# Kernel tuning notes

Hardware: AMD Instinct MI355X
Metric: run time of the kernel (lower is better)

## Reference

```python
import jax, jax.numpy as jnp
import numpy as np

EMBED_DIM = 1024
NUM_HEADS = 16
HEAD_DIM = EMBED_DIM // NUM_HEADS
B, L = 2, 2048
SCALE = HEAD_DIM ** -0.5


def setup_inputs() -> dict:
    key = jax.random.key(0)
    ks = jax.random.split(key, 8)
    x = jax.random.normal(ks[0], (B, L, EMBED_DIM), dtype=jnp.float32)
    phylo_dists = jax.random.uniform(ks[1], (B, L), dtype=jnp.float32)
    alibi_bias = jax.random.normal(ks[2], (NUM_HEADS, L, L), dtype=jnp.float32) * 0.02
    # causal mask: 1 where attending allowed (j <= i), broadcast over B,H
    attn_mask = (jnp.arange(L)[:, None] >= jnp.arange(L)[None, :])[None, None]
    # learned params (Linear stores weight as [out, in]; y = x @ W.T + b)
    qkv_w = jax.random.normal(ks[3], (3 * EMBED_DIM, EMBED_DIM), dtype=jnp.float32) * (EMBED_DIM ** -0.5)
    qkv_b = jnp.zeros((3 * EMBED_DIM,), dtype=jnp.float32)
    out_w = jax.random.normal(ks[4], (EMBED_DIM, EMBED_DIM), dtype=jnp.float32) * (EMBED_DIM ** -0.5)
    out_b = jnp.zeros((EMBED_DIM,), dtype=jnp.float32)
    phylo_alpha = jnp.float32(0.5)
    return {"x": x, "phylo_dists": phylo_dists, "alibi_bias": alibi_bias,
            "attn_mask": attn_mask, "qkv_w": qkv_w, "qkv_b": qkv_b,
            "out_w": out_w, "out_b": out_b, "phylo_alpha": phylo_alpha}


def reference(x, phylo_dists, alibi_bias, attn_mask, qkv_w, qkv_b, out_w, out_b, phylo_alpha):
    Bm, Lm, D = x.shape
    qkv = (x @ qkv_w.T + qkv_b).reshape(Bm, Lm, 3, NUM_HEADS, HEAD_DIM)
    qkv = jnp.transpose(qkv, (2, 0, 3, 1, 4))  # [3, B, H, L, hd]
    q, k, v = qkv[0], qkv[1], qkv[2]
    # phylo temperature: scalar per batch element
    phylo_scalar = phylo_dists.mean(axis=-1).reshape(Bm, 1, 1, 1)
    temp = jnp.clip(1.0 + phylo_alpha * phylo_scalar, 1e-6, None)
    scores = jnp.einsum('bhqd,bhkd->bhqk', q, k) * (SCALE * temp)
    scores = scores + alibi_bias[None]  # [B,H,L,L]
    scores = jnp.where(attn_mask, scores, -jnp.inf)
    attn = jax.nn.softmax(scores, axis=-1)
    out = jnp.einsum('bhqk,bhkd->bhqd', attn, v)
    out = jnp.transpose(out, (0, 2, 1, 3)).reshape(Bm, Lm, D)
    return out @ out_w.T + out_b
```

## Files before the change

### kernel.cpp

```cpp
#include <hip/hip_runtime.h>
#include <hip/hip_bf16.h>

typedef __attribute__((ext_vector_type(8))) short bf16x8;
typedef __attribute__((ext_vector_type(4))) float f32x4;
typedef __attribute__((ext_vector_type(4))) float f4v;
typedef __attribute__((ext_vector_type(4))) short s4v;

__device__ __forceinline__ short f2bf(float f) {
    union { __hip_bfloat16 h; short s; } u;
    u.h = __float2bfloat16(f);
    return u.s;
}

__device__ __forceinline__ void gload_lds16(const void* g, void* l) {
    __builtin_amdgcn_global_load_lds(
        (const __attribute__((address_space(1))) void*)g,
        (__attribute__((address_space(3))) void*)l,
        16, 0, 0);
}

#define MFMA16(a, b, c) __builtin_amdgcn_mfma_f32_16x16x32_bf16((a), (b), (c), 0, 0, 0)

__global__ void prep_kernel(const float* __restrict__ x,
                            const float* __restrict__ qw,
                            const float* __restrict__ ow,
                            const float* __restrict__ pd,
                            const float* __restrict__ alphap,
                            s4v* __restrict__ xb, s4v* __restrict__ qb,
                            s4v* __restrict__ ob, float* __restrict__ scales) {
    __shared__ float wsum[4];
    if (blockIdx.x >= 2048) {
        int b = blockIdx.x - 2048;
        float s = 0.f;
        for (int i = threadIdx.x; i < 2048; i += 256) s += pd[b * 2048 + i];
        for (int o = 32; o; o >>= 1) s += __shfl_down(s, o);
        if ((threadIdx.x & 63) == 0) wsum[threadIdx.x >> 6] = s;
        __syncthreads();
        if (threadIdx.x == 0) {
            float t = wsum[0] + wsum[1] + wsum[2] + wsum[3];
            float mean = t * (1.0f / 2048.0f);
            float temp = fmaxf(1.0f + alphap[0] * mean, 1e-6f);
            scales[b] = 0.125f * temp;
        }
        return;
    }
    #pragma unroll
    for (int j = 0; j < 4; ++j) {
        int idx = blockIdx.x * 1024 + j * 256 + threadIdx.x;
        const f4v* src;
        s4v* dst;
        int off;
        if (idx < 1048576)      { src = (const f4v*)x;  dst = xb; off = idx; }
        else if (idx < 1835008) { src = (const f4v*)qw; dst = qb; off = idx - 1048576; }
        else                    { src = (const f4v*)ow; dst = ob; off = idx - 1835008; }
        f4v v = src[off];
        s4v o;
        #pragma unroll
        for (int k = 0; k < 4; ++k) o[k] = f2bf(v[k]);
        dst[off] = o;
    }
}

__global__ __launch_bounds__(512, 2)
void gemm_qkv_8ph(const __hip_bfloat16* __restrict__ A,
                  const __hip_bfloat16* __restrict__ Bw,
                  const float* __restrict__ bias,
                  __hip_bfloat16* __restrict__ C) {
    extern __shared__ short lds[];
    const int tid = threadIdx.x;
    const int wave = tid >> 6, lane = tid & 63;
    const int g = lane >> 4, c = lane & 15;
    const int wr = wave >> 2, wc = wave & 3;

    int bid = blockIdx.y * 12 + blockIdx.x;
    bid = (bid & 7) * 24 + (bid >> 3);
    const long m0 = (long)(bid / 12) * 256;
    const long n0 = (long)(bid % 12) * 256;

    const int sr = tid >> 3;
    const int ss = tid & 7;
    const int sl = ss ^ (sr & 7);
    const int srowoff = 2 * sr + (sl >> 2);
    const int skel = (sl & 3) * 8;

    const int xterm = (((c & 1) << 6) | (g << 4)) ^ ((c >> 1) << 4);

    f32x4 acc[8][4];
    #pragma unroll
    for (int m = 0; m < 8; ++m)
        #pragma unroll
        for (int n = 0; n < 4; ++n) acc[m][n] = f32x4{0.f, 0.f, 0.f, 0.f};

#define STAGE_A(tt, d)                                                        \
    {                                                                         \
        _Pragma("unroll")                                                     \
        for (int h = 0; h < 2; ++h) {                                         \
            const __hip_bfloat16* src =                                       \
                A + (m0 + h * 128 + srowoff) * 1024 + (tt) * 32 + skel;       \
            gload_lds16(src, lds + (d) * 16384 + (h * 512 + tid) * 8);        \
        }                                                                     \
    }
#define STAGE_B(tt, d)                                                        \
    {                                                                         \
        _Pragma("unroll")                                                     \
        for (int h = 0; h < 2; ++h) {                                         \
            const __hip_bfloat16* src =                                       \
                Bw + (n0 + h * 128 + srowoff) * 1024 + (tt) * 32 + skel;      \
            gload_lds16(src, lds + (d) * 16384 + 8192 + (h * 512 + tid) * 8); \
        }                                                                     \
    }

    STAGE_A(0, 0); STAGE_B(0, 0);
    STAGE_A(1, 1); STAGE_B(1, 1);
    asm volatile("s_waitcnt vmcnt(4)" ::: "memory");
    __builtin_amdgcn_s_barrier();

    const int NT = 32;
    for (int t = 0; t < NT; ++t) {
        const int d = t % 3;
        const char* bufA = (const char*)(lds + d * 16384);
        const char* bufB = (const char*)(lds + d * 16384 + 8192);
        const int dn = (t + 2) % 3;
        const bool st = (t + 2 < NT);

        bf16x8 af[8], bfr0, bfr1;
        #pragma unroll
        for (int m = 0; m < 8; ++m) {
            int row = wr * 64 + m * 8 + (c >> 1);
            af[m] = *(const bf16x8*)(bufA + row * 128 + xterm);
        }
        {
            int row0 = wc * 32 + 0 * 8 + (c >> 1);
            int row1 = wc * 32 + 1 * 8 + (c >> 1);
            bfr0 = *(const bf16x8*)(bufB + row0 * 128 + xterm);
            bfr1 = *(const bf16x8*)(bufB + row1 * 128 + xterm);
        }
        if (st) STAGE_A(t + 2, dn);
        __builtin_amdgcn_s_barrier();
        asm volatile("s_waitcnt lgkmcnt(0)" ::: "memory");
        __builtin_amdgcn_sched_barrier(0);
        __builtin_amdgcn_s_setprio(1);
        #pragma unroll
        for (int m = 0; m < 8; ++m) {
            acc[m][0] = MFMA16(af[m], bfr0, acc[m][0]);
            acc[m][1] = MFMA16(af[m], bfr1, acc[m][1]);
        }
        __builtin_amdgcn_s_setprio(0);
        __builtin_amdgcn_s_barrier();

        {
            int row2 = wc * 32 + 2 * 8 + (c >> 1);
            int row3 = wc * 32 + 3 * 8 + (c >> 1);
            bfr0 = *(const bf16x8*)(bufB + row2 * 128 + xterm);
            bfr1 = *(const bf16x8*)(bufB + row3 * 128 + xterm);
        }
        if (st) STAGE_B(t + 2, dn);
        __builtin_amdgcn_s_barrier();
        if (t < NT - 2)
            asm volatile("s_waitcnt vmcnt(4)" ::: "memory");
        else if (t == NT - 2)
            asm volatile("s_waitcnt vmcnt(0)" ::: "memory");
        asm volatile("s_waitcnt lgkmcnt(0)" ::: "memory");
        __builtin_amdgcn_sched_barrier(0);
        __builtin_amdgcn_s_setprio(1);
        #pragma unroll
        for (int m = 0; m < 8; ++m) {
            acc[m][2] = MFMA16(af[m], bfr0, acc[m][2]);
            acc[m][3] = MFMA16(af[m], bfr1, acc[m][3]);
        }
        __builtin_amdgcn_s_setprio(0);
        __builtin_amdgcn_s_barrier();
    }
#undef STAGE_A
#undef STAGE_B

    #pragma unroll
    for (int m = 0; m < 8; ++m) {
        #pragma unroll
        for (int n = 0; n < 4; ++n) {
            long col = n0 + wc * 64 + n * 16 + c;
            float bv = bias[col];
            #pragma unroll
            for (int r = 0; r < 4; ++r) {
                long row = m0 + wr * 128 + m * 16 + g * 4 + r;
                C[row * 3072 + col] = __float2bfloat16(acc[m][n][r] + bv);
            }
        }
    }
}

template<int BF16_OUT, int NF>
__global__ __launch_bounds__(256, 2)
void gemm_nt(const __hip_bfloat16* __restrict__ A,
             const __hip_bfloat16* __restrict__ Bw,
             const float* __restrict__ bias,
             void* __restrict__ Cv,
             int M, int N, int K) {
    __shared__ short sA[128 * 64];
    __shared__ short sB[NF * 32 * 64];
    const int tid = threadIdx.x;
    const int wave = tid >> 6, lane = tid & 63;
    const int g = lane >> 4, c = lane & 15;
    const int wr = wave >> 1, wc = wave & 1;
    const long m0 = (long)blockIdx.y * 128, n0 = (long)blockIdx.x * (NF * 32);

    f32x4 acc[4][NF];
    #pragma unroll
    for (int m = 0; m < 4; ++m)
        #pragma unroll
        for (int n = 0; n < NF; ++n) acc[m][n] = f32x4{0.f, 0.f, 0.f, 0.f};

    for (int k0 = 0; k0 < K; k0 += 64) {
        #pragma unroll
        for (int i = 0; i < 4; ++i) {
            int cb = (i * 4 + wave) * 64;
            int chunk = cb + lane;
            int row = chunk >> 3;
            int sc = ((chunk & 7) * 16) ^ ((row & 7) << 4);
            const char* gA = (const char*)(A + (m0 + row) * (long)K + k0) + sc;
            gload_lds16(gA, (char*)sA + cb * 16);
        }
        #pragma unroll
        for (int i = 0; i < NF; ++i) {
            int cb = (i * 4 + wave) * 64;
            int chunk = cb + lane;
            int row = chunk >> 3;
            int sc = ((chunk & 7) * 16) ^ ((row & 7) << 4);
            const char* gB = (const char*)(Bw + (n0 + row) * (long)K + k0) + sc;
            gload_lds16(gB, (char*)sB + cb * 16);
        }
        __syncthreads();
        #pragma unroll
        for (int s = 0; s < 2; ++s) {
            bf16x8 af[4], bfr[NF];
            #pragma unroll
            for (int m = 0; m < 4; ++m) {
                int row = wr * 64 + m * 16 + c;
                int kb = (s * 64 + g * 16) ^ ((row & 7) << 4);
                af[m] = *(const bf16x8*)((const char*)sA + row * 128 + kb);
            }
            #pragma unroll
            for (int n = 0; n < NF; ++n) {
                int row = wc * (NF * 16) + n * 16 + c;
                int kb = (s * 64 + g * 16) ^ ((row & 7) << 4);
                bfr[n] = *(const bf16x8*)((const char*)sB + row * 128 + kb);
            }
            #pragma unroll
            for (int m = 0; m < 4; ++m)
                #pragma unroll
                for (int n = 0; n < NF; ++n)
                    acc[m][n] = MFMA16(af[m], bfr[n], acc[m][n]);
        }
        __syncthreads();
    }

    #pragma unroll
    for (int m = 0; m < 4; ++m) {
        #pragma unroll
        for (int n = 0; n < NF; ++n) {
            long col = n0 + wc * (NF * 16) + n * 16 + c;
            float bv = bias[col];
            #pragma unroll
            for (int r = 0; r < 4; ++r) {
                long row = m0 + wr * 64 + m * 16 + g * 4 + r;
                float v = acc[m][n][r] + bv;
                if (BF16_OUT)
                    ((__hip_bfloat16*)Cv)[row * N + col] = __float2bfloat16(v);
                else
                    ((float*)Cv)[row * N + col] = v;
            }
        }
    }
}

__device__ __forceinline__ void compute_tile(
    const bf16x8 (&kf)[4][2], const short* sVtc, short* sPw,
    bf16x8 qf0, bf16x8 qf1,
    f32x4 (&acc_o)[4], f32x4& accL, float (&m)[4],
    const float (&ab)[4][4],
    float scale, int qi0, int kv0, bool diag, int g, int c)
{
    f32x4 accs[4];
    __builtin_amdgcn_s_setprio(1);
    #pragma unroll
    for (int nf = 0; nf < 4; ++nf) {
        accs[nf] = f32x4{0.f, 0.f, 0.f, 0.f};
        accs[nf] = MFMA16(qf0, kf[nf][0], accs[nf]);
        accs[nf] = MFMA16(qf1, kf[nf][1], accs[nf]);
    }
    __builtin_amdgcn_s_setprio(0);
    float s[4][4], pmax[4];
    bool ok = true;
    #pragma unroll
    for (int r = 0; r < 4; ++r) {
        int qi = qi0 + r;
        #pragma unroll
        for (int nf = 0; nf < 4; ++nf) {
            float sv = fmaf(accs[nf][r], scale, ab[nf][r]);
            if (diag && (kv0 + nf * 16 + c > qi)) sv = -1e30f;
            s[r][nf] = sv;
        }
        pmax[r] = fmaxf(fmaxf(s[r][0], s[r][1]), fmaxf(s[r][2], s[r][3]));
        ok = ok && (pmax[r] <= m[r] + 8.0f);
    }
    if (!__all(ok)) {
        #pragma unroll
        for (int r = 0; r < 4; ++r) {
            float mx = pmax[r];
            mx = fmaxf(mx, __shfl_xor(mx, 1));
            mx = fmaxf(mx, __shfl_xor(mx, 2));
            mx = fmaxf(mx, __shfl_xor(mx, 4));
            mx = fmaxf(mx, __shfl_xor(mx, 8));
            float mn = fmaxf(m[r], mx);
            float alpha = __expf(m[r] - mn);
            m[r] = mn;
            accL[r] *= alpha;
            #pragma unroll
            for (int d = 0; d < 4; ++d) acc_o[d][r] *= alpha;
        }
    }
    #pragma unroll
    for (int r = 0; r < 4; ++r)
        #pragma unroll
        for (int nf = 0; nf < 4; ++nf)
            sPw[(g * 4 + r) * 72 + nf * 16 + c] = f2bf(__expf(s[r][nf] - m[r]));
    asm volatile("s_waitcnt lgkmcnt(0)" ::: "memory");
    bf16x8 pf0 = *(const bf16x8*)((const char*)sPw + c * 144 + g * 16);
    bf16x8 pf1 = *(const bf16x8*)((const char*)sPw + c * 144 + 64 + g * 16);
    const short ONE = 0x3F80;
    const bf16x8 ones = {ONE, ONE, ONE, ONE, ONE, ONE, ONE, ONE};
    __builtin_amdgcn_s_setprio(1);
    accL = MFMA16(pf0, ones, accL);
    accL = MFMA16(pf1, ones, accL);
    #pragma unroll
    for (int d = 0; d < 4; ++d) {
        const char* vb = (const char*)sVtc + (d * 16 + c) * 144;
        bf16x8 vf0 = *(const bf16x8*)(vb + g * 16);
        bf16x8 vf1 = *(const bf16x8*)(vb + 64 + g * 16);
        acc_o[d] = MFMA16(pf0, vf0, acc_o[d]);
        acc_o[d] = MFMA16(pf1, vf1, acc_o[d]);
    }
    __builtin_amdgcn_s_setprio(0);
}

__global__ __launch_bounds__(256, 2)
void attn_kernel(const __hip_bfloat16* __restrict__ qkv,
                 const float* __restrict__ alibi,
                 const float* __restrict__ scales,
                 __hip_bfloat16* __restrict__ out) {
    __shared__ short sK[2][64 * 64];
    __shared__ short sVt[2][64 * 72];
    __shared__ short sPA[4][16 * 72];
    __shared__ short sPB[4][16 * 72];

    const int p = blockIdx.x, h = blockIdx.y, b = blockIdx.z;
    const int qtA = p, qtB = 31 - p;
    const int nIter = qtB + 1;
    const int tid = threadIdx.x;
    const int wave = tid >> 6, lane = tid & 63;
    const int g = lane >> 4, c = lane & 15;
    const float scale = scales[b];
    const long base_bl = (long)b * 2048;

    const int qA0 = qtA * 64 + wave * 16;
    const int qB0 = qtB * 64 + wave * 16;

    const __hip_bfloat16* qrowA = qkv + (base_bl + qA0 + c) * 3072 + h * 64;
    const __hip_bfloat16* qrowB = qkv + (base_bl + qB0 + c) * 3072 + h * 64;
    bf16x8 qAf0 = *(const bf16x8*)(qrowA + g * 8);
    bf16x8 qAf1 = *(const bf16x8*)(qrowA + 32 + g * 8);
    bf16x8 qBf0 = *(const bf16x8*)(qrowB + g * 8);
    bf16x8 qBf1 = *(const bf16x8*)(qrowB + 32 + g * 8);

    const __hip_bfloat16* kg = qkv + base_bl * 3072 + 1024 + h * 64;
    const __hip_bfloat16* vg = qkv + base_bl * 3072 + 2048 + h * 64;
    const float* abA_base = alibi + (long)h * 2048 * 2048 + (long)(qA0 + g * 4) * 2048;
    const float* abB_base = alibi + (long)h * 2048 * 2048 + (long)(qB0 + g * 4) * 2048;

    const int p2 = tid & 31;
    const int d0 = (tid >> 5) * 8;
    const __hip_bfloat16* vrow = vg + (long)(2 * p2) * 3072 + d0;

    f32x4 accA[4], accB[4], accLA, accLB;
    float mA[4], mB[4];
    #pragma unroll
    for (int d = 0; d < 4; ++d) {
        accA[d] = f32x4{0.f, 0.f, 0.f, 0.f};
        accB[d] = f32x4{0.f, 0.f, 0.f, 0.f};
    }
    accLA = f32x4{0.f, 0.f, 0.f, 0.f};
    accLB = f32x4{0.f, 0.f, 0.f, 0.f};
    #pragma unroll
    for (int r = 0; r < 4; ++r) { mA[r] = -3e38f; mB[r] = -3e38f; }

    float abA[4][4], abB[4][4], abAn[4][4], abBn[4][4];

    {
        #pragma unroll
        for (int i = 0; i < 2; ++i) {
            int cb = (i * 4 + wave) * 64;
            int chunk = cb + lane;
            int row = chunk >> 3;
            int sc = ((chunk & 7) * 16) ^ ((row & 7) << 4);
            gload_lds16((const char*)(kg + (long)row * 3072) + sc,
                        (char*)sK[0] + cb * 16);
        }
        bf16x8 va = *(const bf16x8*)vrow;
        bf16x8 vb = *(const bf16x8*)(vrow + 3072);
        #pragma unroll
        for (int j = 0; j < 8; ++j) {
            unsigned pk = ((unsigned)(unsigned short)va[j]) |
                          (((unsigned)(unsigned short)vb[j]) << 16);
            *(unsigned*)((char*)sVt[0] + (d0 + j) * 144 + p2 * 4) = pk;
        }
        #pragma unroll
        for (int nf = 0; nf < 4; ++nf)
            #pragma unroll
            for (int r = 0; r < 4; ++r) {
                abA[nf][r] = abA_base[(long)r * 2048 + nf * 16 + c];
                abB[nf][r] = abB_base[(long)r * 2048 + nf * 16 + c];
                abAn[nf][r] = 0.f; abBn[nf][r] = 0.f;
            }
    }
    __syncthreads();

    for (int t = 0; t < nIter; ++t) {
        const int cur = t & 1;
        const int kv0 = t * 64;
        bf16x8 va, vb;
        const bool haveNext = (t + 1 < nIter);
        if (haveNext) {
            #pragma unroll
            for (int i = 0; i < 2; ++i) {
                int cb = (i * 4 + wave) * 64;
                int chunk = cb + lane;
                int row = chunk >> 3;
                int sc = ((chunk & 7) * 16) ^ ((row & 7) << 4);
                gload_lds16((const char*)(kg + (long)(kv0 + 64 + row) * 3072) + sc,
                            (char*)sK[cur ^ 1] + cb * 16);
            }
            const __hip_bfloat16* vp = vrow + (long)(kv0 + 64) * 3072;
            va = *(const bf16x8*)vp;
            vb = *(const bf16x8*)(vp + 3072);
            #pragma unroll
            for (int nf = 0; nf < 4; ++nf)
                #pragma unroll
                for (int r = 0; r < 4; ++r)
                    abBn[nf][r] = abB_base[(long)r * 2048 + kv0 + 64 + nf * 16 + c];
        }
        if (t + 1 <= qtA) {
            #pragma unroll
            for (int nf = 0; nf < 4; ++nf)
                #pragma unroll
                for (int r = 0; r < 4; ++r)
                    abAn[nf][r] = abA_base[(long)r * 2048 + kv0 + 64 + nf * 16 + c];
        }

        bf16x8 kf[4][2];
        const int swz = (c & 7) << 4;
        #pragma unroll
        for (int nf = 0; nf < 4; ++nf) {
            const char* kb = (const char*)sK[cur] + (nf * 16 + c) * 128;
            kf[nf][0] = *(const bf16x8*)(kb + ((g * 16) ^ swz));
            kf[nf][1] = *(const bf16x8*)(kb + ((64 + g * 16) ^ swz));
        }

        compute_tile(kf, sVt[cur], &sPB[wave][0], qBf0, qBf1,
                     accB, accLB, mB, abB, scale, qB0 + g * 4, kv0, t == qtB, g, c);
        if (t <= qtA)
            compute_tile(kf, sVt[cur], &sPA[wave][0], qAf0, qAf1,
                         accA, accLA, mA, abA, scale, qA0 + g * 4, kv0, t == qtA, g, c);

        if (haveNext) {
            #pragma unroll
            for (int j = 0; j < 8; ++j) {
                unsigned pk = ((unsigned)(unsigned short)va[j]) |
                              (((unsigned)(unsigned short)vb[j]) << 16);
                *(unsigned*)((char*)sVt[cur ^ 1] + (d0 + j) * 144 + p2 * 4) = pk;
            }
        }
        __syncthreads();
        #pragma unroll
        for (int nf = 0; nf < 4; ++nf)
            #pragma unroll
            for (int r = 0; r < 4; ++r) {
                abA[nf][r] = abAn[nf][r];
                abB[nf][r] = abBn[nf][r];
            }
    }

    __hip_bfloat16* opA = out + (base_bl + qA0 + g * 4) * 1024 + h * 64;
    __hip_bfloat16* opB = out + (base_bl + qB0 + g * 4) * 1024 + h * 64;
    #pragma unroll
    for (int r = 0; r < 4; ++r) {
        float invA = 1.0f / accLA[r];
        float invB = 1.0f / accLB[r];
        #pragma unroll
        for (int d = 0; d < 4; ++d) {
            opA[(long)r * 1024 + d * 16 + c] = __float2bfloat16(accA[d][r] * invA);
            opB[(long)r * 1024 + d * 16 + c] = __float2bfloat16(accB[d][r] * invB);
        }
    }
}

extern "C" void kernel_launch(void* const* d_in, const int* in_sizes, int n_in,
                              void* d_out, int out_size, void* d_ws, size_t ws_size,
                              hipStream_t stream) {
    const float* x      = (const float*)d_in[0];
    const float* phylo  = (const float*)d_in[1];
    const float* alibi  = (const float*)d_in[2];
    const float* qkv_w  = (const float*)d_in[4];
    const float* qkv_b  = (const float*)d_in[5];
    const float* out_w  = (const float*)d_in[6];
    const float* out_b  = (const float*)d_in[7];
    const float* alphap = (const float*)d_in[8];

    char* ws = (char*)d_ws;
    __hip_bfloat16* xbf   = (__hip_bfloat16*)(ws);
    __hip_bfloat16* qwbf  = (__hip_bfloat16*)(ws + (8l << 20));
    __hip_bfloat16* owbf  = (__hip_bfloat16*)(ws + (14l << 20));
    __hip_bfloat16* qkvbf = (__hip_bfloat16*)(ws + (16l << 20));
    __hip_bfloat16* aobf  = (__hip_bfloat16*)(ws + (40l << 20));
    float* scales         = (float*)(ws + (48l << 20));

    (void)hipFuncSetAttribute((const void*)gemm_qkv_8ph,
                              hipFuncAttributeMaxDynamicSharedMemorySize, 98304);

    prep_kernel<<<2050, 256, 0, stream>>>(x, qkv_w, out_w, phylo, alphap,
                                          (s4v*)xbf, (s4v*)qwbf, (s4v*)owbf, scales);

    gemm_qkv_8ph<<<dim3(12, 16), 512, 98304, stream>>>(xbf, qwbf, qkv_b, qkvbf);
    attn_kernel<<<dim3(16, 16, 2), 256, 0, stream>>>(qkvbf, alibi, scales, aobf);
    gemm_nt<0, 2><<<dim3(16, 32), 256, 0, stream>>>(aobf, owbf, out_b, d_out,
                                                    4096, 1024, 1024);
}
```

Baseline: 136.7 us.

## Software-pipeline PV of previous tile with QK of current tile in attention

Splits the per-tile attention step into softmax-and-store and PV-accumulate phases. The PV MFMAs for tile t-1 are issued alongside the QK MFMAs for tile t, so matrix work can hide the latency of the softmax and LDS round-trips. To support this, the P buffers are double-buffered, V is triple-buffered, and the last tile's PV is drained after the loop. Padded LDS rows are replaced with XOR-swizzled 128-byte rows. Shared memory per block grows, which may limit occupancy.

```diff
diff --git a/kernel.cpp b/kernel.cpp
--- a/kernel.cpp
+++ b/kernel.cpp
@@ -273,22 +273,12 @@
     }
 }
 
-__device__ __forceinline__ void compute_tile(
-    const bf16x8 (&kf)[4][2], const short* sVtc, short* sPw,
-    bf16x8 qf0, bf16x8 qf1,
-    f32x4 (&acc_o)[4], f32x4& accL, float (&m)[4],
-    const float (&ab)[4][4],
+
+__device__ __forceinline__ void softmax_store(
+    const f32x4 (&accs)[4], const float (&ab)[4][4], float (&m)[4],
+    f32x4& accL, f32x4 (&acc_o)[4], short* sPw,
     float scale, int qi0, int kv0, bool diag, int g, int c)
 {
-    f32x4 accs[4];
-    __builtin_amdgcn_s_setprio(1);
-    #pragma unroll
-    for (int nf = 0; nf < 4; ++nf) {
-        accs[nf] = f32x4{0.f, 0.f, 0.f, 0.f};
-        accs[nf] = MFMA16(qf0, kf[nf][0], accs[nf]);
-        accs[nf] = MFMA16(qf1, kf[nf][1], accs[nf]);
-    }
-    __builtin_amdgcn_s_setprio(0);
     float s[4][4], pmax[4];
     bool ok = true;
     #pragma unroll
@@ -320,27 +310,35 @@
         }
     }
     #pragma unroll
-    for (int r = 0; r < 4; ++r)
+    for (int r = 0; r < 4; ++r) {
+        int row = g * 4 + r;
         #pragma unroll
         for (int nf = 0; nf < 4; ++nf)
-            sPw[(g * 4 + r) * 72 + nf * 16 + c] = f2bf(__expf(s[r][nf] - m[r]));
-    asm volatile("s_waitcnt lgkmcnt(0)" ::: "memory");
-    bf16x8 pf0 = *(const bf16x8*)((const char*)sPw + c * 144 + g * 16);
-    bf16x8 pf1 = *(const bf16x8*)((const char*)sPw + c * 144 + 64 + g * 16);
+            *(short*)((char*)sPw + row * 128 +
+                      ((nf * 32 + c * 2) ^ ((row & 7) << 4))) =
+                f2bf(__expf(s[r][nf] - m[r]));
+    }
+}
+
+__device__ __forceinline__ void pv_accum(
+    const short* sPw, const short* sVtc,
+    f32x4 (&acc_o)[4], f32x4& accL, int g, int c)
+{
+    const int cs = (c & 7) << 4;
+    bf16x8 pf0 = *(const bf16x8*)((const char*)sPw + c * 128 + ((g * 16) ^ cs));
+    bf16x8 pf1 = *(const bf16x8*)((const char*)sPw + c * 128 + ((64 + g * 16) ^ cs));
     const short ONE = 0x3F80;
     const bf16x8 ones = {ONE, ONE, ONE, ONE, ONE, ONE, ONE, ONE};
-    __builtin_amdgcn_s_setprio(1);
     accL = MFMA16(pf0, ones, accL);
     accL = MFMA16(pf1, ones, accL);
     #pragma unroll
     for (int d = 0; d < 4; ++d) {
-        const char* vb = (const char*)sVtc + (d * 16 + c) * 144;
-        bf16x8 vf0 = *(const bf16x8*)(vb + g * 16);
-        bf16x8 vf1 = *(const bf16x8*)(vb + 64 + g * 16);
+        const char* vb = (const char*)sVtc + (d * 16 + c) * 128;
+        bf16x8 vf0 = *(const bf16x8*)(vb + ((g * 16) ^ cs));
+        bf16x8 vf1 = *(const bf16x8*)(vb + ((64 + g * 16) ^ cs));
         acc_o[d] = MFMA16(pf0, vf0, acc_o[d]);
         acc_o[d] = MFMA16(pf1, vf1, acc_o[d]);
     }
-    __builtin_amdgcn_s_setprio(0);
 }
 
 __global__ __launch_bounds__(256, 2)
@@ -349,9 +347,9 @@
                  const float* __restrict__ scales,
                  __hip_bfloat16* __restrict__ out) {
     __shared__ short sK[2][64 * 64];
-    __shared__ short sVt[2][64 * 72];
-    __shared__ short sPA[4][16 * 72];
-    __shared__ short sPB[4][16 * 72];
+    __shared__ short sVt[3][64 * 64];
+    __shared__ short sPB[4][2][16 * 64];
+    __shared__ short sPA[4][2][16 * 64];
 
     const int p = blockIdx.x, h = blockIdx.y, b = blockIdx.z;
     const int qtA = p, qtB = 31 - p;
@@ -409,9 +407,11 @@
         bf16x8 vb = *(const bf16x8*)(vrow + 3072);
         #pragma unroll
         for (int j = 0; j < 8; ++j) {
+            int row = d0 + j;
             unsigned pk = ((unsigned)(unsigned short)va[j]) |
                           (((unsigned)(unsigned short)vb[j]) << 16);
-            *(unsigned*)((char*)sVt[0] + (d0 + j) * 144 + p2 * 4) = pk;
+            *(unsigned*)((char*)sVt[0] + row * 128 +
+                         ((p2 * 4) ^ ((row & 7) << 4))) = pk;
         }
         #pragma unroll
         for (int nf = 0; nf < 4; ++nf)
@@ -425,10 +425,11 @@
     __syncthreads();
 
     for (int t = 0; t < nIter; ++t) {
-        const int cur = t & 1;
         const int kv0 = t * 64;
+        const bool haveNext = (t + 1 < nIter);
+        const bool dualT = (t <= qtA);
         bf16x8 va, vb;
-        const bool haveNext = (t + 1 < nIter);
+
         if (haveNext) {
             #pragma unroll
             for (int i = 0; i < 2; ++i) {
@@ -437,7 +438,7 @@
                 int row = chunk >> 3;
                 int sc = ((chunk & 7) * 16) ^ ((row & 7) << 4);
                 gload_lds16((const char*)(kg + (long)(kv0 + 64 + row) * 3072) + sc,
-                            (char*)sK[cur ^ 1] + cb * 16);
+                            (char*)sK[(t + 1) & 1] + cb * 16);
             }
             const __hip_bfloat16* vp = vrow + (long)(kv0 + 64) * 3072;
             va = *(const bf16x8*)vp;
@@ -460,23 +461,52 @@
         const int swz = (c & 7) << 4;
         #pragma unroll
         for (int nf = 0; nf < 4; ++nf) {
-            const char* kb = (const char*)sK[cur] + (nf * 16 + c) * 128;
+            const char* kb = (const char*)sK[t & 1] + (nf * 16 + c) * 128;
             kf[nf][0] = *(const bf16x8*)(kb + ((g * 16) ^ swz));
             kf[nf][1] = *(const bf16x8*)(kb + ((64 + g * 16) ^ swz));
         }
 
-        compute_tile(kf, sVt[cur], &sPB[wave][0], qBf0, qBf1,
-                     accB, accLB, mB, abB, scale, qB0 + g * 4, kv0, t == qtB, g, c);
-        if (t <= qtA)
-            compute_tile(kf, sVt[cur], &sPA[wave][0], qAf0, qAf1,
-                         accA, accLA, mA, abA, scale, qA0 + g * 4, kv0, t == qtA, g, c);
+        f32x4 accsB[4];
+        __builtin_amdgcn_s_setprio(1);
+        #pragma unroll
+        for (int nf = 0; nf < 4; ++nf) {
+            accsB[nf] = f32x4{0.f, 0.f, 0.f, 0.f};
+            accsB[nf] = MFMA16(qBf0, kf[nf][0], accsB[nf]);
+            accsB[nf] = MFMA16(qBf1, kf[nf][1], accsB[nf]);
+        }
+        if (t >= 1) {
+            const short* sVp = sVt[(t - 1) % 3];
+            pv_accum(&sPB[wave][(t - 1) & 1][0], sVp, accB, accLB, g, c);
+            if (t - 1 <= qtA)
+                pv_accum(&sPA[wave][(t - 1) & 1][0], sVp, accA, accLA, g, c);
+        }
+        __builtin_amdgcn_s_setprio(0);
+
+        softmax_store(accsB, abB, mB, accLB, accB, &sPB[wave][t & 1][0],
+                      scale, qB0 + g * 4, kv0, t == qtB, g, c);
+
+        if (dualT) {
+            f32x4 accsA[4];
+            __builtin_amdgcn_s_setprio(1);
+            #pragma unroll
+            for (int nf = 0; nf < 4; ++nf) {
+                accsA[nf] = f32x4{0.f, 0.f, 0.f, 0.f};
+                accsA[nf] = MFMA16(qAf0, kf[nf][0], accsA[nf]);
+                accsA[nf] = MFMA16(qAf1, kf[nf][1], accsA[nf]);
+            }
+            __builtin_amdgcn_s_setprio(0);
+            softmax_store(accsA, abA, mA, accLA, accA, &sPA[wave][t & 1][0],
+                          scale, qA0 + g * 4, kv0, t == qtA, g, c);
+        }
 
         if (haveNext) {
+            char* sVn = (char*)sVt[(t + 1) % 3];
             #pragma unroll
             for (int j = 0; j < 8; ++j) {
+                int row = d0 + j;
                 unsigned pk = ((unsigned)(unsigned short)va[j]) |
                               (((unsigned)(unsigned short)vb[j]) << 16);
-                *(unsigned*)((char*)sVt[cur ^ 1] + (d0 + j) * 144 + p2 * 4) = pk;
+                *(unsigned*)(sVn + row * 128 + ((p2 * 4) ^ ((row & 7) << 4))) = pk;
             }
         }
         __syncthreads();
@@ -488,6 +518,9 @@
                 abB[nf][r] = abBn[nf][r];
             }
     }
+
+    pv_accum(&sPB[wave][(nIter - 1) & 1][0], sVt[(nIter - 1) % 3],
+             accB, accLB, g, c);
 
     __hip_bfloat16* opA = out + (base_bl + qA0 + g * 4) * 1024 + h * 64;
     __hip_bfloat16* opB = out + (base_bl + qB0 + g * 4) * 1024 + h * 64;
```

Measured after the change: 240.5 us. +75.9%, slower.
